# Optimization experiments

Hardware: AMD Instinct MI355X
Metric: run time of the kernel (lower is better)

The kernel has to match this reference:

```python
import jax, jax.numpy as jnp
import numpy as np

N_NODES = 100000
N_EDGES = 3200000
IN_F, HID, OUT = 3, 32, 1
NEG_SLOPE = 0.2


def _glorot(key, shape):
    fan_in, fan_out = shape[0], shape[-1]
    lim = jnp.sqrt(6.0 / (fan_in + fan_out)).astype(jnp.float32)
    return jax.random.uniform(key, shape, jnp.float32, -lim, lim)


def setup_inputs() -> dict:
    key = jax.random.key(0)
    ks = jax.random.split(key, 12)
    x = jax.random.normal(ks[0], (N_NODES, IN_F), jnp.float32)
    edge_index = jax.random.randint(ks[1], (2, N_EDGES), 0, N_NODES, jnp.int32)
    return {
        "x": x,
        "edge_index": edge_index,
        "W1": _glorot(ks[2], (IN_F, HID)),
        "att_src1": _glorot(ks[3], (1, HID))[0],
        "att_dst1": _glorot(ks[4], (1, HID))[0],
        "b1": jnp.zeros((HID,), jnp.float32),
        "W2": _glorot(ks[5], (HID, HID)),
        "att_src2": _glorot(ks[6], (1, HID))[0],
        "att_dst2": _glorot(ks[7], (1, HID))[0],
        "b2": jnp.zeros((HID,), jnp.float32),
        "Wl": _glorot(ks[8], (HID, OUT)),
        "bl": jnp.zeros((OUT,), jnp.float32),
    }


def gat_layer(x, src, dst, W, att_src, att_dst, b):
    # h: [N, HID] dense transform
    h = x @ W
    # per-node attention halves (compute once per node, gather per edge)
    a_s = h @ att_src  # [N]
    a_d = h @ att_dst  # [N]
    logits = jax.nn.leaky_relu(a_s[src] + a_d[dst], NEG_SLOPE)  # [E+N]
    # segment-softmax over incoming edges of each dst node
    m = jax.ops.segment_max(logits, dst, num_segments=N_NODES)
    m = jnp.where(jnp.isfinite(m), m, 0.0)
    ex = jnp.exp(logits - m[dst])
    denom = jax.ops.segment_sum(ex, dst, num_segments=N_NODES)
    coef = ex / (denom[dst] + 1e-16)
    # weighted scatter-aggregate of source messages
    out = jax.ops.segment_sum(coef[:, None] * h[src], dst, num_segments=N_NODES)
    return out + b


def reference(x, edge_index, W1, att_src1, att_dst1, b1, W2, att_src2, att_dst2, b2, Wl, bl):
    # PyG GATConv default: add self-loops
    loops = jnp.arange(N_NODES, dtype=edge_index.dtype)
    src = jnp.concatenate([edge_index[0], loops])
    dst = jnp.concatenate([edge_index[1], loops])
    h = gat_layer(x, src, dst, W1, att_src1, att_dst1, b1)
    h = jax.nn.relu(h)  # dropout is identity in eval
    h = gat_layer(h, src, dst, W2, att_src2, att_dst2, b2)
    h = jax.nn.relu(h)
    return h @ Wl + bl
```

## Files before the change

kernel.cpp:

```cpp
#include <hip/hip_runtime.h>
#include <hip/hip_fp16.h>

#define HID 32
#define BN 132
#define NBPAD 768
#define BSTRIDE 5120
#define CHUNK 4096

__device__ __forceinline__ float lrelu(float x) { return x > 0.0f ? x : 0.2f * x; }

__global__ void k_transform1(const float* __restrict__ x,
                             const float* __restrict__ W1,
                             const float* __restrict__ att_src,
                             const float* __restrict__ att_dst,
                             __half* __restrict__ hh,
                             float* __restrict__ a_s,
                             float* __restrict__ a_d,
                             int* __restrict__ cursor,
                             int N)
{
    int tid = blockIdx.x * blockDim.x + threadIdx.x;
    if (tid < NBPAD) cursor[tid] = 0;
    int n = tid >> 5;
    int f = tid & 31;
    if (n >= N) return;
    float x0 = x[n * 3 + 0], x1 = x[n * 3 + 1], x2 = x[n * 3 + 2];
    float hv = x0 * W1[f] + x1 * W1[HID + f] + x2 * W1[2 * HID + f];
    hh[(size_t)n * HID + f] = __float2half(hv);
    float as = hv * att_src[f];
    float ad = hv * att_dst[f];
    #pragma unroll
    for (int m = 16; m >= 1; m >>= 1) {
        as += __shfl_xor(as, m, 32);
        ad += __shfl_xor(ad, m, 32);
    }
    if (f == 0) { a_s[n] = as; a_d[n] = ad; }
}

__global__ void __launch_bounds__(256) k_binscatter(const int* __restrict__ src,
                                                    const int* __restrict__ dst,
                                                    int* __restrict__ cursor,
                                                    unsigned int* __restrict__ packed,
                                                    int NBr, int E)
{
    __shared__ int stage[CHUNK];
    __shared__ unsigned short sbid[CHUNK];
    __shared__ int lhist[NBPAD], lexcl[NBPAD], lbase[NBPAD], lcur[NBPAD];
    __shared__ int arr[256];
    int t = threadIdx.x;
    for (int i = t; i < NBPAD; i += 256) { lhist[i] = 0; lcur[i] = 0; }
    __syncthreads();
    int base = blockIdx.x * CHUNK;
    int cnt = E - base; if (cnt > CHUNK) cnt = CHUNK;
    for (int i = t; i < cnt; i += 256)
        atomicAdd(&lhist[dst[base + i] / BN], 1);
    __syncthreads();
    int b0 = 3 * t;
    int c0 = lhist[b0], c1 = lhist[b0 + 1], c2 = lhist[b0 + 2];
    int s = c0 + c1 + c2;
    arr[t] = s;
    __syncthreads();
    for (int o = 1; o < 256; o <<= 1) {
        int v = (t >= o) ? arr[t - o] : 0;
        __syncthreads();
        arr[t] += v;
        __syncthreads();
    }
    int ex = arr[t] - s;
    int e0 = ex, e1 = ex + c0, e2 = ex + c0 + c1;
    lexcl[b0] = e0; lexcl[b0 + 1] = e1; lexcl[b0 + 2] = e2;
    for (int i = 0; i < c0; ++i) sbid[e0 + i] = (unsigned short)b0;
    for (int i = 0; i < c1; ++i) sbid[e1 + i] = (unsigned short)(b0 + 1);
    for (int i = 0; i < c2; ++i) sbid[e2 + i] = (unsigned short)(b0 + 2);
    for (int b = t; b < NBr; b += 256)
        if (lhist[b]) lbase[b] = b * BSTRIDE + atomicAdd(&cursor[b], lhist[b]);
    __syncthreads();
    for (int i = t; i < cnt; i += 256) {
        int d = dst[base + i];
        int sv = src[base + i];
        int b = d / BN;
        int dl = d - b * BN;
        int idx = lexcl[b] + atomicAdd(&lcur[b], 1);
        stage[idx] = (int)((unsigned)sv | ((unsigned)dl << 17));
    }
    __syncthreads();
    for (int i = t; i < cnt; i += 256) {
        int b = sbid[i];
        int gpos = lbase[b] + (i - lexcl[b]);
        if (gpos < (b + 1) * BSTRIDE)
            packed[gpos] = (unsigned)stage[i];
    }
}

__device__ __forceinline__ void build_lcsr_exp(const unsigned int* pk, int cnt,
                                               const float* __restrict__ a_s,
                                               const float* __restrict__ a_d,
                                               int nodeBase, int N,
                                               int* lcsr, float* lexp, float* adT,
                                               int* lhist, int* lscan, int* lcur)
{
    int t = threadIdx.x;
    if (t < 256) { lhist[t] = 0; lcur[t] = 0; }
    if (t < BN) {
        int n = nodeBase + t;
        adT[t] = (n < N) ? a_d[n] : 0.0f;
    }
    __syncthreads();
    for (int i = t; i < cnt; i += 512)
        atomicAdd(&lhist[(pk[i] >> 17) & 255], 1);
    __syncthreads();
    if (t < 256) lscan[t] = lhist[t];
    __syncthreads();
    for (int o = 1; o < 256; o <<= 1) {
        int v = (t < 256 && t >= o) ? lscan[t - o] : 0;
        __syncthreads();
        if (t < 256) lscan[t] += v;
        __syncthreads();
    }
    for (int i = t; i < cnt; i += 512) {
        unsigned int p = pk[i];
        int dl = (p >> 17) & 255;
        int sv = (int)(p & 0x1FFFF);
        float e = __expf(lrelu(a_s[sv] + adT[dl]));
        int pos = atomicAdd(&lcur[dl], 1);
        int idx = (lscan[dl] - lhist[dl]) + pos;
        lcsr[idx] = sv;
        lexp[idx] = e;
    }
    __syncthreads();
}

__device__ __forceinline__ void agg_node(const __half* __restrict__ hh,
                                         float ex_self,
                                         const float* __restrict__ b,
                                         int n, int f,
                                         const int* lcsr, const float* lexp,
                                         int off, int dg,
                                         float& vx, float& vy)
{
    float den = ex_self;
    float2 hs = __half22float2(*(const __half2*)(hh + (size_t)n * HID + 2 * f));
    float accx = ex_self * hs.x;
    float accy = ex_self * hs.y;
    int j = 0;
    for (; j + 8 <= dg; j += 8) {
        int s0 = lcsr[off + j + 0], s1 = lcsr[off + j + 1];
        int s2 = lcsr[off + j + 2], s3 = lcsr[off + j + 3];
        int s4 = lcsr[off + j + 4], s5 = lcsr[off + j + 5];
        int s6 = lcsr[off + j + 6], s7 = lcsr[off + j + 7];
        float e0 = lexp[off + j + 0], e1 = lexp[off + j + 1];
        float e2 = lexp[off + j + 2], e3 = lexp[off + j + 3];
        float e4 = lexp[off + j + 4], e5 = lexp[off + j + 5];
        float e6 = lexp[off + j + 6], e7 = lexp[off + j + 7];
        __half2 p0 = *(const __half2*)(hh + (size_t)s0 * HID + 2 * f);
        __half2 p1 = *(const __half2*)(hh + (size_t)s1 * HID + 2 * f);
        __half2 p2 = *(const __half2*)(hh + (size_t)s2 * HID + 2 * f);
        __half2 p3 = *(const __half2*)(hh + (size_t)s3 * HID + 2 * f);
        __half2 p4 = *(const __half2*)(hh + (size_t)s4 * HID + 2 * f);
        __half2 p5 = *(const __half2*)(hh + (size_t)s5 * HID + 2 * f);
        __half2 p6 = *(const __half2*)(hh + (size_t)s6 * HID + 2 * f);
        __half2 p7 = *(const __half2*)(hh + (size_t)s7 * HID + 2 * f);
        float2 q0 = __half22float2(p0), q1 = __half22float2(p1);
        float2 q2 = __half22float2(p2), q3 = __half22float2(p3);
        float2 q4 = __half22float2(p4), q5 = __half22float2(p5);
        float2 q6 = __half22float2(p6), q7 = __half22float2(p7);
        den += ((e0 + e1) + (e2 + e3)) + ((e4 + e5) + (e6 + e7));
        accx = fmaf(e0, q0.x, accx); accy = fmaf(e0, q0.y, accy);
        accx = fmaf(e1, q1.x, accx); accy = fmaf(e1, q1.y, accy);
        accx = fmaf(e2, q2.x, accx); accy = fmaf(e2, q2.y, accy);
        accx = fmaf(e3, q3.x, accx); accy = fmaf(e3, q3.y, accy);
        accx = fmaf(e4, q4.x, accx); accy = fmaf(e4, q4.y, accy);
        accx = fmaf(e5, q5.x, accx); accy = fmaf(e5, q5.y, accy);
        accx = fmaf(e6, q6.x, accx); accy = fmaf(e6, q6.y, accy);
        accx = fmaf(e7, q7.x, accx); accy = fmaf(e7, q7.y, accy);
    }
    for (; j < dg; ++j) {
        int s0 = lcsr[off + j];
        float e0 = lexp[off + j];
        float2 q0 = __half22float2(*(const __half2*)(hh + (size_t)s0 * HID + 2 * f));
        den += e0;
        accx = fmaf(e0, q0.x, accx);
        accy = fmaf(e0, q0.y, accy);
    }
    float inv = 1.0f / (den + 1e-16f);
    vx = fmaxf(accx * inv + b[2 * f], 0.0f);
    vy = fmaxf(accy * inv + b[2 * f + 1], 0.0f);
}

__global__ void __launch_bounds__(512) k_agg_mid_f(const __half* __restrict__ hh,
                          const float* __restrict__ a_s,
                          const float* __restrict__ a_d,
                          const int* __restrict__ cursor,
                          const unsigned int* __restrict__ packed,
                          const float* __restrict__ b1,
                          const float* __restrict__ W2,
                          const float* __restrict__ as2w,
                          const float* __restrict__ ad2w,
                          __half* __restrict__ hh_out,
                          float* __restrict__ as_out,
                          float* __restrict__ ad_out,
                          int N)
{
    __shared__ int lcsr[BSTRIDE];
    __shared__ float lexp[BSTRIDE];
    __shared__ float adT[BN];
    __shared__ int lhist[256], lscan[256], lcur[256];
    int bk = blockIdx.x, t = threadIdx.x;
    int cnt = cursor[bk]; if (cnt > BSTRIDE) cnt = BSTRIDE;
    build_lcsr_exp(packed + (size_t)bk * BSTRIDE, cnt, a_s, a_d, bk * BN, N,
                   lcsr, lexp, adT, lhist, lscan, lcur);
    int g = t >> 4, f = t & 15;
    for (int dl = g; dl < BN; dl += 32) {
        int n = bk * BN + dl;
        if (n >= N) continue;
        int off = lscan[dl] - lhist[dl];
        int dg = lhist[dl];
        float ex_self = __expf(lrelu(a_s[n] + adT[dl]));
        float vx, vy;
        agg_node(hh, ex_self, b1, n, f, lcsr, lexp, off, dg, vx, vy);
        float hx = 0.0f, hy = 0.0f;
        #pragma unroll
        for (int k = 0; k < 16; ++k) {
            float va = __shfl(vx, k, 16);
            float vb = __shfl(vy, k, 16);
            float2 w0 = *(const float2*)(W2 + (2 * k) * HID + 2 * f);
            float2 w1 = *(const float2*)(W2 + (2 * k + 1) * HID + 2 * f);
            hx = fmaf(va, w0.x, hx); hy = fmaf(va, w0.y, hy);
            hx = fmaf(vb, w1.x, hx); hy = fmaf(vb, w1.y, hy);
        }
        *(__half2*)(hh_out + (size_t)n * HID + 2 * f) = __floats2half2_rn(hx, hy);
        float as = hx * as2w[2 * f] + hy * as2w[2 * f + 1];
        float ad = hx * ad2w[2 * f] + hy * ad2w[2 * f + 1];
        #pragma unroll
        for (int m2 = 8; m2 >= 1; m2 >>= 1) {
            as += __shfl_xor(as, m2, 16);
            ad += __shfl_xor(ad, m2, 16);
        }
        if (f == 0) { as_out[n] = as; ad_out[n] = ad; }
    }
}

__global__ void __launch_bounds__(512) k_agg_out_f(const __half* __restrict__ hh,
                          const float* __restrict__ a_s,
                          const float* __restrict__ a_d,
                          const int* __restrict__ cursor,
                          const unsigned int* __restrict__ packed,
                          const float* __restrict__ b2,
                          const float* __restrict__ Wl,
                          const float* __restrict__ bl,
                          float* __restrict__ out,
                          int N)
{
    __shared__ int lcsr[BSTRIDE];
    __shared__ float lexp[BSTRIDE];
    __shared__ float adT[BN];
    __shared__ int lhist[256], lscan[256], lcur[256];
    int bk = blockIdx.x, t = threadIdx.x;
    int cnt = cursor[bk]; if (cnt > BSTRIDE) cnt = BSTRIDE;
    build_lcsr_exp(packed + (size_t)bk * BSTRIDE, cnt, a_s, a_d, bk * BN, N,
                   lcsr, lexp, adT, lhist, lscan, lcur);
    int g = t >> 4, f = t & 15;
    for (int dl = g; dl < BN; dl += 32) {
        int n = bk * BN + dl;
        if (n >= N) continue;
        int off = lscan[dl] - lhist[dl];
        int dg = lhist[dl];
        float ex_self = __expf(lrelu(a_s[n] + adT[dl]));
        float vx, vy;
        agg_node(hh, ex_self, b2, n, f, lcsr, lexp, off, dg, vx, vy);
        float y = vx * Wl[2 * f] + vy * Wl[2 * f + 1];
        #pragma unroll
        for (int m2 = 8; m2 >= 1; m2 >>= 1)
            y += __shfl_xor(y, m2, 16);
        if (f == 0) out[n] = y + bl[0];
    }
}

extern "C" void kernel_launch(void* const* d_in, const int* in_sizes, int n_in,
                              void* d_out, int out_size, void* d_ws, size_t ws_size,
                              hipStream_t stream)
{
    const float* x        = (const float*)d_in[0];
    const int*   eidx     = (const int*)d_in[1];
    const float* W1       = (const float*)d_in[2];
    const float* att_src1 = (const float*)d_in[3];
    const float* att_dst1 = (const float*)d_in[4];
    const float* b1       = (const float*)d_in[5];
    const float* W2       = (const float*)d_in[6];
    const float* att_src2 = (const float*)d_in[7];
    const float* att_dst2 = (const float*)d_in[8];
    const float* b2       = (const float*)d_in[9];
    const float* Wl       = (const float*)d_in[10];
    const float* bl       = (const float*)d_in[11];
    float* out = (float*)d_out;

    int N = in_sizes[0] / 3;
    int E = in_sizes[1] / 2;
    const int* src = eidx;
    const int* dst = eidx + E;
    int NBr = (N + BN - 1) / BN;

    size_t szNHh = (size_t)N * HID * 2;
    size_t szN4  = (size_t)N * 4;
    size_t szPK  = (size_t)NBr * BSTRIDE * 4;

    char* ws = (char*)d_ws;
    __half* h1h    = (__half*)ws; ws += szNHh;
    __half* h2h    = (__half*)ws; ws += szNHh;
    unsigned int* packed = (unsigned int*)ws; ws += szPK;
    float*  a_s1   = (float*)ws;  ws += szN4;
    float*  a_d1   = (float*)ws;  ws += szN4;
    float*  a_s2   = (float*)ws;  ws += szN4;
    float*  a_d2   = (float*)ws;  ws += szN4;
    int*    cursor = (int*)ws;    ws += NBPAD * 4;

    const int B = 256;
    int gridNode32 = (N * HID + B - 1) / B;
    int gridBin    = (E + CHUNK - 1) / CHUNK;

    k_transform1<<<gridNode32, B, 0, stream>>>(x, W1, att_src1, att_dst1,
                                               h1h, a_s1, a_d1, cursor, N);
    k_binscatter<<<gridBin, B, 0, stream>>>(src, dst, cursor, packed, NBr, E);
    k_agg_mid_f<<<NBr, 512, 0, stream>>>(h1h, a_s1, a_d1, cursor, packed,
                                         b1, W2, att_src2, att_dst2,
                                         h2h, a_s2, a_d2, N);
    k_agg_out_f<<<NBr, 512, 0, stream>>>(h2h, a_s2, a_d2, cursor, packed,
                                         b2, Wl, bl, out, N);
}
```

Baseline: 252.3 us.

## Split node features into two half-width arrays and gather in two passes

Stores the 32-wide fp16 hidden features as two separate 16-wide arrays and runs the aggregation as two sequential gather passes, one per half. Partial sums for the first half are kept in shared memory between the passes. The aim is to shrink the working set of each random gather pass (3.2 MB per half) so it stays cache-resident, and to use 8 lanes per node instead of 16. In exchange, the edge list is walked twice per layer, each gather fetches only 32 bytes per row, and the extra shared memory may lower occupancy.

```diff
diff --git a/kernel.cpp b/kernel.cpp
--- a/kernel.cpp
+++ b/kernel.cpp
@@ -2,6 +2,7 @@
 #include <hip/hip_fp16.h>
 
 #define HID 32
+#define HHALF 16
 #define BN 132
 #define NBPAD 768
 #define BSTRIDE 5120
@@ -13,7 +14,8 @@
                              const float* __restrict__ W1,
                              const float* __restrict__ att_src,
                              const float* __restrict__ att_dst,
-                             __half* __restrict__ hh,
+                             __half* __restrict__ hhA,
+                             __half* __restrict__ hhB,
                              float* __restrict__ a_s,
                              float* __restrict__ a_d,
                              int* __restrict__ cursor,
@@ -26,7 +28,8 @@
     if (n >= N) return;
     float x0 = x[n * 3 + 0], x1 = x[n * 3 + 1], x2 = x[n * 3 + 2];
     float hv = x0 * W1[f] + x1 * W1[HID + f] + x2 * W1[2 * HID + f];
-    hh[(size_t)n * HID + f] = __float2half(hv);
+    if (f < HHALF) hhA[(size_t)n * HHALF + f] = __float2half(hv);
+    else           hhB[(size_t)n * HHALF + (f - HHALF)] = __float2half(hv);
     float as = hv * att_src[f];
     float ad = hv * att_dst[f];
     #pragma unroll
@@ -130,18 +133,18 @@
     __syncthreads();
 }
 
-__device__ __forceinline__ void agg_node(const __half* __restrict__ hh,
-                                         float ex_self,
-                                         const float* __restrict__ b,
-                                         int n, int f,
-                                         const int* lcsr, const float* lexp,
-                                         int off, int dg,
-                                         float& vx, float& vy)
-{
-    float den = ex_self;
-    float2 hs = __half22float2(*(const __half2*)(hh + (size_t)n * HID + 2 * f));
-    float accx = ex_self * hs.x;
-    float accy = ex_self * hs.y;
+__device__ __forceinline__ void gather_half(const __half* __restrict__ hhX,
+                                            const int* lcsr, const float* lexp,
+                                            int off, int dg, int f,
+                                            float ex_self, int n,
+                                            bool accDen,
+                                            float& ax, float& ay, float& den)
+{
+    __half2 hs = *(const __half2*)(hhX + (size_t)n * HHALF + 2 * f);
+    float2 q = __half22float2(hs);
+    ax = ex_self * q.x;
+    ay = ex_self * q.y;
+    float d = accDen ? ex_self : 0.0f;
     int j = 0;
     for (; j + 8 <= dg; j += 8) {
         int s0 = lcsr[off + j + 0], s1 = lcsr[off + j + 1];
@@ -152,42 +155,41 @@
         float e2 = lexp[off + j + 2], e3 = lexp[off + j + 3];
         float e4 = lexp[off + j + 4], e5 = lexp[off + j + 5];
         float e6 = lexp[off + j + 6], e7 = lexp[off + j + 7];
-        __half2 p0 = *(const __half2*)(hh + (size_t)s0 * HID + 2 * f);
-        __half2 p1 = *(const __half2*)(hh + (size_t)s1 * HID + 2 * f);
-        __half2 p2 = *(const __half2*)(hh + (size_t)s2 * HID + 2 * f);
-        __half2 p3 = *(const __half2*)(hh + (size_t)s3 * HID + 2 * f);
-        __half2 p4 = *(const __half2*)(hh + (size_t)s4 * HID + 2 * f);
-        __half2 p5 = *(const __half2*)(hh + (size_t)s5 * HID + 2 * f);
-        __half2 p6 = *(const __half2*)(hh + (size_t)s6 * HID + 2 * f);
-        __half2 p7 = *(const __half2*)(hh + (size_t)s7 * HID + 2 * f);
+        __half2 p0 = *(const __half2*)(hhX + (size_t)s0 * HHALF + 2 * f);
+        __half2 p1 = *(const __half2*)(hhX + (size_t)s1 * HHALF + 2 * f);
+        __half2 p2 = *(const __half2*)(hhX + (size_t)s2 * HHALF + 2 * f);
+        __half2 p3 = *(const __half2*)(hhX + (size_t)s3 * HHALF + 2 * f);
+        __half2 p4 = *(const __half2*)(hhX + (size_t)s4 * HHALF + 2 * f);
+        __half2 p5 = *(const __half2*)(hhX + (size_t)s5 * HHALF + 2 * f);
+        __half2 p6 = *(const __half2*)(hhX + (size_t)s6 * HHALF + 2 * f);
+        __half2 p7 = *(const __half2*)(hhX + (size_t)s7 * HHALF + 2 * f);
         float2 q0 = __half22float2(p0), q1 = __half22float2(p1);
         float2 q2 = __half22float2(p2), q3 = __half22float2(p3);
         float2 q4 = __half22float2(p4), q5 = __half22float2(p5);
         float2 q6 = __half22float2(p6), q7 = __half22float2(p7);
-        den += ((e0 + e1) + (e2 + e3)) + ((e4 + e5) + (e6 + e7));
-        accx = fmaf(e0, q0.x, accx); accy = fmaf(e0, q0.y, accy);
-        accx = fmaf(e1, q1.x, accx); accy = fmaf(e1, q1.y, accy);
-        accx = fmaf(e2, q2.x, accx); accy = fmaf(e2, q2.y, accy);
-        accx = fmaf(e3, q3.x, accx); accy = fmaf(e3, q3.y, accy);
-        accx = fmaf(e4, q4.x, accx); accy = fmaf(e4, q4.y, accy);
-        accx = fmaf(e5, q5.x, accx); accy = fmaf(e5, q5.y, accy);
-        accx = fmaf(e6, q6.x, accx); accy = fmaf(e6, q6.y, accy);
-        accx = fmaf(e7, q7.x, accx); accy = fmaf(e7, q7.y, accy);
+        if (accDen) d += ((e0 + e1) + (e2 + e3)) + ((e4 + e5) + (e6 + e7));
+        ax = fmaf(e0, q0.x, ax); ay = fmaf(e0, q0.y, ay);
+        ax = fmaf(e1, q1.x, ax); ay = fmaf(e1, q1.y, ay);
+        ax = fmaf(e2, q2.x, ax); ay = fmaf(e2, q2.y, ay);
+        ax = fmaf(e3, q3.x, ax); ay = fmaf(e3, q3.y, ay);
+        ax = fmaf(e4, q4.x, ax); ay = fmaf(e4, q4.y, ay);
+        ax = fmaf(e5, q5.x, ax); ay = fmaf(e5, q5.y, ay);
+        ax = fmaf(e6, q6.x, ax); ay = fmaf(e6, q6.y, ay);
+        ax = fmaf(e7, q7.x, ax); ay = fmaf(e7, q7.y, ay);
     }
     for (; j < dg; ++j) {
         int s0 = lcsr[off + j];
         float e0 = lexp[off + j];
-        float2 q0 = __half22float2(*(const __half2*)(hh + (size_t)s0 * HID + 2 * f));
-        den += e0;
-        accx = fmaf(e0, q0.x, accx);
-        accy = fmaf(e0, q0.y, accy);
-    }
-    float inv = 1.0f / (den + 1e-16f);
-    vx = fmaxf(accx * inv + b[2 * f], 0.0f);
-    vy = fmaxf(accy * inv + b[2 * f + 1], 0.0f);
-}
-
-__global__ void __launch_bounds__(512) k_agg_mid_f(const __half* __restrict__ hh,
+        float2 q0 = __half22float2(*(const __half2*)(hhX + (size_t)s0 * HHALF + 2 * f));
+        if (accDen) d += e0;
+        ax = fmaf(e0, q0.x, ax);
+        ay = fmaf(e0, q0.y, ay);
+    }
+    if (accDen) den = d;
+}
+
+__global__ void __launch_bounds__(512) k_agg_mid_f(const __half* __restrict__ hhA,
+                          const __half* __restrict__ hhB,
                           const float* __restrict__ a_s,
                           const float* __restrict__ a_d,
                           const int* __restrict__ cursor,
@@ -196,7 +198,8 @@
                           const float* __restrict__ W2,
                           const float* __restrict__ as2w,
                           const float* __restrict__ ad2w,
-                          __half* __restrict__ hh_out,
+                          __half* __restrict__ hhA_out,
+                          __half* __restrict__ hhB_out,
                           float* __restrict__ as_out,
                           float* __restrict__ ad_out,
                           int N)
@@ -204,43 +207,81 @@
     __shared__ int lcsr[BSTRIDE];
     __shared__ float lexp[BSTRIDE];
     __shared__ float adT[BN];
+    __shared__ float accA[BN * HHALF];
+    __shared__ float denB[BN];
     __shared__ int lhist[256], lscan[256], lcur[256];
     int bk = blockIdx.x, t = threadIdx.x;
     int cnt = cursor[bk]; if (cnt > BSTRIDE) cnt = BSTRIDE;
     build_lcsr_exp(packed + (size_t)bk * BSTRIDE, cnt, a_s, a_d, bk * BN, N,
                    lcsr, lexp, adT, lhist, lscan, lcur);
-    int g = t >> 4, f = t & 15;
-    for (int dl = g; dl < BN; dl += 32) {
+    int g = t >> 3, f = t & 7;
+    for (int dl = g; dl < BN; dl += 64) {
         int n = bk * BN + dl;
         if (n >= N) continue;
         int off = lscan[dl] - lhist[dl];
         int dg = lhist[dl];
-        float ex_self = __expf(lrelu(a_s[n] + adT[dl]));
-        float vx, vy;
-        agg_node(hh, ex_self, b1, n, f, lcsr, lexp, off, dg, vx, vy);
-        float hx = 0.0f, hy = 0.0f;
+        float exs = __expf(lrelu(a_s[n] + adT[dl]));
+        float ax, ay, den;
+        gather_half(hhA, lcsr, lexp, off, dg, f, exs, n, true, ax, ay, den);
+        accA[dl * HHALF + 2 * f] = ax;
+        accA[dl * HHALF + 2 * f + 1] = ay;
+        if (f == 0) denB[dl] = den;
+    }
+    __syncthreads();
+    for (int dl = g; dl < BN; dl += 64) {
+        int n = bk * BN + dl;
+        if (n >= N) continue;
+        int off = lscan[dl] - lhist[dl];
+        int dg = lhist[dl];
+        float exs = __expf(lrelu(a_s[n] + adT[dl]));
+        float bx, by, dummy;
+        gather_half(hhB, lcsr, lexp, off, dg, f, exs, n, false, bx, by, dummy);
+        float inv = 1.0f / (denB[dl] + 1e-16f);
+        float vAx = fmaxf(accA[dl * HHALF + 2 * f] * inv + b1[2 * f], 0.0f);
+        float vAy = fmaxf(accA[dl * HHALF + 2 * f + 1] * inv + b1[2 * f + 1], 0.0f);
+        float vBx = fmaxf(bx * inv + b1[HHALF + 2 * f], 0.0f);
+        float vBy = fmaxf(by * inv + b1[HHALF + 2 * f + 1], 0.0f);
+        float oAx = 0.0f, oAy = 0.0f, oBx = 0.0f, oBy = 0.0f;
         #pragma unroll
-        for (int k = 0; k < 16; ++k) {
-            float va = __shfl(vx, k, 16);
-            float vb = __shfl(vy, k, 16);
-            float2 w0 = *(const float2*)(W2 + (2 * k) * HID + 2 * f);
-            float2 w1 = *(const float2*)(W2 + (2 * k + 1) * HID + 2 * f);
-            hx = fmaf(va, w0.x, hx); hy = fmaf(va, w0.y, hy);
-            hx = fmaf(vb, w1.x, hx); hy = fmaf(vb, w1.y, hy);
+        for (int r = 0; r < 8; ++r) {
+            float k0 = __shfl(vAx, r, 8);
+            float k1 = __shfl(vAy, r, 8);
+            float k2 = __shfl(vBx, r, 8);
+            float k3 = __shfl(vBy, r, 8);
+            const float* w0 = W2 + (2 * r) * HID;
+            const float* w1 = W2 + (2 * r + 1) * HID;
+            const float* w2 = W2 + (HHALF + 2 * r) * HID;
+            const float* w3 = W2 + (HHALF + 2 * r + 1) * HID;
+            float2 a0 = *(const float2*)(w0 + 2 * f), c0 = *(const float2*)(w0 + HHALF + 2 * f);
+            float2 a1 = *(const float2*)(w1 + 2 * f), c1 = *(const float2*)(w1 + HHALF + 2 * f);
+            float2 a2 = *(const float2*)(w2 + 2 * f), c2 = *(const float2*)(w2 + HHALF + 2 * f);
+            float2 a3 = *(const float2*)(w3 + 2 * f), c3 = *(const float2*)(w3 + HHALF + 2 * f);
+            oAx = fmaf(k0, a0.x, oAx); oAy = fmaf(k0, a0.y, oAy);
+            oBx = fmaf(k0, c0.x, oBx); oBy = fmaf(k0, c0.y, oBy);
+            oAx = fmaf(k1, a1.x, oAx); oAy = fmaf(k1, a1.y, oAy);
+            oBx = fmaf(k1, c1.x, oBx); oBy = fmaf(k1, c1.y, oBy);
+            oAx = fmaf(k2, a2.x, oAx); oAy = fmaf(k2, a2.y, oAy);
+            oBx = fmaf(k2, c2.x, oBx); oBy = fmaf(k2, c2.y, oBy);
+            oAx = fmaf(k3, a3.x, oAx); oAy = fmaf(k3, a3.y, oAy);
+            oBx = fmaf(k3, c3.x, oBx); oBy = fmaf(k3, c3.y, oBy);
         }
-        *(__half2*)(hh_out + (size_t)n * HID + 2 * f) = __floats2half2_rn(hx, hy);
-        float as = hx * as2w[2 * f] + hy * as2w[2 * f + 1];
-        float ad = hx * ad2w[2 * f] + hy * ad2w[2 * f + 1];
+        *(__half2*)(hhA_out + (size_t)n * HHALF + 2 * f) = __floats2half2_rn(oAx, oAy);
+        *(__half2*)(hhB_out + (size_t)n * HHALF + 2 * f) = __floats2half2_rn(oBx, oBy);
+        float as = oAx * as2w[2 * f] + oAy * as2w[2 * f + 1]
+                 + oBx * as2w[HHALF + 2 * f] + oBy * as2w[HHALF + 2 * f + 1];
+        float ad = oAx * ad2w[2 * f] + oAy * ad2w[2 * f + 1]
+                 + oBx * ad2w[HHALF + 2 * f] + oBy * ad2w[HHALF + 2 * f + 1];
         #pragma unroll
-        for (int m2 = 8; m2 >= 1; m2 >>= 1) {
-            as += __shfl_xor(as, m2, 16);
-            ad += __shfl_xor(ad, m2, 16);
+        for (int m2 = 4; m2 >= 1; m2 >>= 1) {
+            as += __shfl_xor(as, m2, 8);
+            ad += __shfl_xor(ad, m2, 8);
         }
         if (f == 0) { as_out[n] = as; ad_out[n] = ad; }
     }
 }
 
-__global__ void __launch_bounds__(512) k_agg_out_f(const __half* __restrict__ hh,
+__global__ void __launch_bounds__(512) k_agg_out_f(const __half* __restrict__ hhA,
+                          const __half* __restrict__ hhB,
                           const float* __restrict__ a_s,
                           const float* __restrict__ a_d,
                           const int* __restrict__ cursor,
@@ -254,24 +295,45 @@
     __shared__ int lcsr[BSTRIDE];
     __shared__ float lexp[BSTRIDE];
     __shared__ float adT[BN];
+    __shared__ float accA[BN * HHALF];
+    __shared__ float denB[BN];
     __shared__ int lhist[256], lscan[256], lcur[256];
     int bk = blockIdx.x, t = threadIdx.x;
     int cnt = cursor[bk]; if (cnt > BSTRIDE) cnt = BSTRIDE;
     build_lcsr_exp(packed + (size_t)bk * BSTRIDE, cnt, a_s, a_d, bk * BN, N,
                    lcsr, lexp, adT, lhist, lscan, lcur);
-    int g = t >> 4, f = t & 15;
-    for (int dl = g; dl < BN; dl += 32) {
+    int g = t >> 3, f = t & 7;
+    for (int dl = g; dl < BN; dl += 64) {
         int n = bk * BN + dl;
         if (n >= N) continue;
         int off = lscan[dl] - lhist[dl];
         int dg = lhist[dl];
-        float ex_self = __expf(lrelu(a_s[n] + adT[dl]));
-        float vx, vy;
-        agg_node(hh, ex_self, b2, n, f, lcsr, lexp, off, dg, vx, vy);
-        float y = vx * Wl[2 * f] + vy * Wl[2 * f + 1];
+        float exs = __expf(lrelu(a_s[n] + adT[dl]));
+        float ax, ay, den;
+        gather_half(hhA, lcsr, lexp, off, dg, f, exs, n, true, ax, ay, den);
+        accA[dl * HHALF + 2 * f] = ax;
+        accA[dl * HHALF + 2 * f + 1] = ay;
+        if (f == 0) denB[dl] = den;
+    }
+    __syncthreads();
+    for (int dl = g; dl < BN; dl += 64) {
+        int n = bk * BN + dl;
+        if (n >= N) continue;
+        int off = lscan[dl] - lhist[dl];
+        int dg = lhist[dl];
+        float exs = __expf(lrelu(a_s[n] + adT[dl]));
+        float bx, by, dummy;
+        gather_half(hhB, lcsr, lexp, off, dg, f, exs, n, false, bx, by, dummy);
+        float inv = 1.0f / (denB[dl] + 1e-16f);
+        float vAx = fmaxf(accA[dl * HHALF + 2 * f] * inv + b2[2 * f], 0.0f);
+        float vAy = fmaxf(accA[dl * HHALF + 2 * f + 1] * inv + b2[2 * f + 1], 0.0f);
+        float vBx = fmaxf(bx * inv + b2[HHALF + 2 * f], 0.0f);
+        float vBy = fmaxf(by * inv + b2[HHALF + 2 * f + 1], 0.0f);
+        float y = vAx * Wl[2 * f] + vAy * Wl[2 * f + 1]
+                + vBx * Wl[HHALF + 2 * f] + vBy * Wl[HHALF + 2 * f + 1];
         #pragma unroll
-        for (int m2 = 8; m2 >= 1; m2 >>= 1)
-            y += __shfl_xor(y, m2, 16);
+        for (int m2 = 4; m2 >= 1; m2 >>= 1)
+            y += __shfl_xor(y, m2, 8);
         if (f == 0) out[n] = y + bl[0];
     }
 }
@@ -300,13 +362,15 @@
     const int* dst = eidx + E;
     int NBr = (N + BN - 1) / BN;
 
-    size_t szNHh = (size_t)N * HID * 2;
+    size_t szNHf = (size_t)N * HHALF * 2;
     size_t szN4  = (size_t)N * 4;
     size_t szPK  = (size_t)NBr * BSTRIDE * 4;
 
     char* ws = (char*)d_ws;
-    __half* h1h    = (__half*)ws; ws += szNHh;
-    __half* h2h    = (__half*)ws; ws += szNHh;
+    __half* h1A    = (__half*)ws; ws += szNHf;
+    __half* h1B    = (__half*)ws; ws += szNHf;
+    __half* h2A    = (__half*)ws; ws += szNHf;
+    __half* h2B    = (__half*)ws; ws += szNHf;
     unsigned int* packed = (unsigned int*)ws; ws += szPK;
     float*  a_s1   = (float*)ws;  ws += szN4;
     float*  a_d1   = (float*)ws;  ws += szN4;
@@ -319,11 +383,11 @@
     int gridBin    = (E + CHUNK - 1) / CHUNK;
 
     k_transform1<<<gridNode32, B, 0, stream>>>(x, W1, att_src1, att_dst1,
-                                               h1h, a_s1, a_d1, cursor, N);
+                                               h1A, h1B, a_s1, a_d1, cursor, N);
     k_binscatter<<<gridBin, B, 0, stream>>>(src, dst, cursor, packed, NBr, E);
-    k_agg_mid_f<<<NBr, 512, 0, stream>>>(h1h, a_s1, a_d1, cursor, packed,
+    k_agg_mid_f<<<NBr, 512, 0, stream>>>(h1A, h1B, a_s1, a_d1, cursor, packed,
                                          b1, W2, att_src2, att_dst2,
-                                         h2h, a_s2, a_d2, N);
-    k_agg_out_f<<<NBr, 512, 0, stream>>>(h2h, a_s2, a_d2, cursor, packed,
+                                         h2A, h2B, a_s2, a_d2, N);
+    k_agg_out_f<<<NBr, 512, 0, stream>>>(h2A, h2B, a_s2, a_d2, cursor, packed,
                                          b2, Wl, bl, out, N);
 }
```

Result: slower. 268.7 us (+6.5%).

## Fuse all GAT stages into one persistent kernel with grid barriers

Applied to the files above, without the earlier changes.

Replaces the four launches (transform, bin-scatter, two aggregation passes) with one persistent kernel of one block per destination bin. The stages are separated by atomic-counter grid barriers, and a host-side occupancy check falls back to the old path if all blocks cannot be co-resident. Layer 2 reuses the shared-memory CSR built in layer 1 and only recomputes the exponentials, locating each edge's destination by binary search, instead of rebuilding the CSR. BN and BSTRIDE are retuned so the bin count fits under NBPAD. This removes launch gaps and the second CSR build, at the cost of 256-thread aggregation blocks, barrier spin overhead, and reliance on all blocks being resident.

```diff
diff --git a/kernel.cpp b/kernel.cpp
--- a/kernel.cpp
+++ b/kernel.cpp
@@ -2,111 +2,89 @@
 #include <hip/hip_fp16.h>
 
 #define HID 32
-#define BN 132
+#define BN 131
 #define NBPAD 768
-#define BSTRIDE 5120
+#define BSTRIDE 4608
 #define CHUNK 4096
 
 __device__ __forceinline__ float lrelu(float x) { return x > 0.0f ? x : 0.2f * x; }
 
-__global__ void k_transform1(const float* __restrict__ x,
-                             const float* __restrict__ W1,
-                             const float* __restrict__ att_src,
-                             const float* __restrict__ att_dst,
-                             __half* __restrict__ hh,
-                             float* __restrict__ a_s,
-                             float* __restrict__ a_d,
-                             int* __restrict__ cursor,
-                             int N)
-{
-    int tid = blockIdx.x * blockDim.x + threadIdx.x;
-    if (tid < NBPAD) cursor[tid] = 0;
-    int n = tid >> 5;
-    int f = tid & 31;
-    if (n >= N) return;
-    float x0 = x[n * 3 + 0], x1 = x[n * 3 + 1], x2 = x[n * 3 + 2];
-    float hv = x0 * W1[f] + x1 * W1[HID + f] + x2 * W1[2 * HID + f];
-    hh[(size_t)n * HID + f] = __float2half(hv);
-    float as = hv * att_src[f];
-    float ad = hv * att_dst[f];
-    #pragma unroll
-    for (int m = 16; m >= 1; m >>= 1) {
-        as += __shfl_xor(as, m, 32);
-        ad += __shfl_xor(ad, m, 32);
-    }
-    if (f == 0) { a_s[n] = as; a_d[n] = ad; }
-}
-
-__global__ void __launch_bounds__(256) k_binscatter(const int* __restrict__ src,
-                                                    const int* __restrict__ dst,
-                                                    int* __restrict__ cursor,
-                                                    unsigned int* __restrict__ packed,
-                                                    int NBr, int E)
-{
-    __shared__ int stage[CHUNK];
-    __shared__ unsigned short sbid[CHUNK];
-    __shared__ int lhist[NBPAD], lexcl[NBPAD], lbase[NBPAD], lcur[NBPAD];
-    __shared__ int arr[256];
+
+struct BinSM {
+    int stage[CHUNK];
+    unsigned short sbid[CHUNK];
+    int lhist[NBPAD], lexcl[NBPAD], lbase[NBPAD], lcur[NBPAD];
+    int arr[256];
+};
+struct AggSM {
+    int   lcsr[BSTRIDE];
+    float lexp[BSTRIDE];
+    int   lhist[256], lscan[256], lcur[256];
+    float adT[BN];
+};
+union FusedSM { BinSM bin; AggSM agg; };
+
+__device__ __forceinline__ void binscatter_chunk(BinSM& S, int base,
+        const int* __restrict__ src, const int* __restrict__ dst,
+        int* __restrict__ cursor, unsigned int* __restrict__ packed,
+        int NBr, int E)
+{
     int t = threadIdx.x;
-    for (int i = t; i < NBPAD; i += 256) { lhist[i] = 0; lcur[i] = 0; }
-    __syncthreads();
-    int base = blockIdx.x * CHUNK;
+    for (int i = t; i < NBPAD; i += 256) { S.lhist[i] = 0; S.lcur[i] = 0; }
+    __syncthreads();
     int cnt = E - base; if (cnt > CHUNK) cnt = CHUNK;
     for (int i = t; i < cnt; i += 256)
-        atomicAdd(&lhist[dst[base + i] / BN], 1);
+        atomicAdd(&S.lhist[dst[base + i] / BN], 1);
     __syncthreads();
     int b0 = 3 * t;
-    int c0 = lhist[b0], c1 = lhist[b0 + 1], c2 = lhist[b0 + 2];
+    int c0 = S.lhist[b0], c1 = S.lhist[b0 + 1], c2 = S.lhist[b0 + 2];
     int s = c0 + c1 + c2;
-    arr[t] = s;
+    S.arr[t] = s;
     __syncthreads();
     for (int o = 1; o < 256; o <<= 1) {
-        int v = (t >= o) ? arr[t - o] : 0;
+        int v = (t >= o) ? S.arr[t - o] : 0;
         __syncthreads();
-        arr[t] += v;
+        S.arr[t] += v;
         __syncthreads();
     }
-    int ex = arr[t] - s;
+    int ex = S.arr[t] - s;
     int e0 = ex, e1 = ex + c0, e2 = ex + c0 + c1;
-    lexcl[b0] = e0; lexcl[b0 + 1] = e1; lexcl[b0 + 2] = e2;
-    for (int i = 0; i < c0; ++i) sbid[e0 + i] = (unsigned short)b0;
-    for (int i = 0; i < c1; ++i) sbid[e1 + i] = (unsigned short)(b0 + 1);
-    for (int i = 0; i < c2; ++i) sbid[e2 + i] = (unsigned short)(b0 + 2);
+    S.lexcl[b0] = e0; S.lexcl[b0 + 1] = e1; S.lexcl[b0 + 2] = e2;
+    for (int i = 0; i < c0; ++i) S.sbid[e0 + i] = (unsigned short)b0;
+    for (int i = 0; i < c1; ++i) S.sbid[e1 + i] = (unsigned short)(b0 + 1);
+    for (int i = 0; i < c2; ++i) S.sbid[e2 + i] = (unsigned short)(b0 + 2);
     for (int b = t; b < NBr; b += 256)
-        if (lhist[b]) lbase[b] = b * BSTRIDE + atomicAdd(&cursor[b], lhist[b]);
+        if (S.lhist[b]) S.lbase[b] = b * BSTRIDE + atomicAdd(&cursor[b], S.lhist[b]);
     __syncthreads();
     for (int i = t; i < cnt; i += 256) {
         int d = dst[base + i];
         int sv = src[base + i];
         int b = d / BN;
         int dl = d - b * BN;
-        int idx = lexcl[b] + atomicAdd(&lcur[b], 1);
-        stage[idx] = (int)((unsigned)sv | ((unsigned)dl << 17));
+        int idx = S.lexcl[b] + atomicAdd(&S.lcur[b], 1);
+        S.stage[idx] = (int)((unsigned)sv | ((unsigned)dl << 17));
     }
     __syncthreads();
     for (int i = t; i < cnt; i += 256) {
-        int b = sbid[i];
-        int gpos = lbase[b] + (i - lexcl[b]);
+        int b = S.sbid[i];
+        int gpos = S.lbase[b] + (i - S.lexcl[b]);
         if (gpos < (b + 1) * BSTRIDE)
-            packed[gpos] = (unsigned)stage[i];
-    }
-}
-
-__device__ __forceinline__ void build_lcsr_exp(const unsigned int* pk, int cnt,
-                                               const float* __restrict__ a_s,
-                                               const float* __restrict__ a_d,
-                                               int nodeBase, int N,
-                                               int* lcsr, float* lexp, float* adT,
-                                               int* lhist, int* lscan, int* lcur)
+            packed[gpos] = (unsigned)S.stage[i];
+    }
+}
+
+template<int BLK>
+__device__ __forceinline__ void build_csr_exp(int* lcsr, float* lexp, float* adT,
+        int* lhist, int* lscan, int* lcur,
+        const unsigned int* __restrict__ pk, int cnt,
+        const float* __restrict__ a_s, const float* __restrict__ a_d,
+        int nodeBase, int N)
 {
     int t = threadIdx.x;
     if (t < 256) { lhist[t] = 0; lcur[t] = 0; }
-    if (t < BN) {
-        int n = nodeBase + t;
-        adT[t] = (n < N) ? a_d[n] : 0.0f;
-    }
-    __syncthreads();
-    for (int i = t; i < cnt; i += 512)
+    if (t < BN) { int n = nodeBase + t; adT[t] = (n < N) ? a_d[n] : 0.0f; }
+    __syncthreads();
+    for (int i = t; i < cnt; i += BLK)
         atomicAdd(&lhist[(pk[i] >> 17) & 255], 1);
     __syncthreads();
     if (t < 256) lscan[t] = lhist[t];
@@ -117,8 +95,8 @@
         if (t < 256) lscan[t] += v;
         __syncthreads();
     }
-    for (int i = t; i < cnt; i += 512) {
-        unsigned int p = pk[i];
+    for (int i = t; i < cnt; i += BLK) {
+        unsigned p = pk[i];
         int dl = (p >> 17) & 255;
         int sv = (int)(p & 0x1FFFF);
         float e = __expf(lrelu(a_s[sv] + adT[dl]));
@@ -131,12 +109,10 @@
 }
 
 __device__ __forceinline__ void agg_node(const __half* __restrict__ hh,
-                                         float ex_self,
-                                         const float* __restrict__ b,
+                                         float ex_self, const float* __restrict__ b,
                                          int n, int f,
                                          const int* lcsr, const float* lexp,
-                                         int off, int dg,
-                                         float& vx, float& vy)
+                                         int off, int dg, float& vx, float& vy)
 {
     float den = ex_self;
     float2 hs = __half22float2(*(const __half2*)(hh + (size_t)n * HID + 2 * f));
@@ -187,87 +163,224 @@
     vy = fmaxf(accy * inv + b[2 * f + 1], 0.0f);
 }
 
+__device__ __forceinline__ void epi_mid(int n, int f, float vx, float vy,
+        const float* __restrict__ W2, const float* __restrict__ as2w,
+        const float* __restrict__ ad2w,
+        __half* __restrict__ hh_out, float* __restrict__ as_out,
+        float* __restrict__ ad_out)
+{
+    float hx = 0.0f, hy = 0.0f;
+    #pragma unroll
+    for (int k = 0; k < 16; ++k) {
+        float va = __shfl(vx, k, 16);
+        float vb = __shfl(vy, k, 16);
+        float2 w0 = *(const float2*)(W2 + (2 * k) * HID + 2 * f);
+        float2 w1 = *(const float2*)(W2 + (2 * k + 1) * HID + 2 * f);
+        hx = fmaf(va, w0.x, hx); hy = fmaf(va, w0.y, hy);
+        hx = fmaf(vb, w1.x, hx); hy = fmaf(vb, w1.y, hy);
+    }
+    *(__half2*)(hh_out + (size_t)n * HID + 2 * f) = __floats2half2_rn(hx, hy);
+    float as = hx * as2w[2 * f] + hy * as2w[2 * f + 1];
+    float ad = hx * ad2w[2 * f] + hy * ad2w[2 * f + 1];
+    #pragma unroll
+    for (int m2 = 8; m2 >= 1; m2 >>= 1) {
+        as += __shfl_xor(as, m2, 16);
+        ad += __shfl_xor(ad, m2, 16);
+    }
+    if (f == 0) { as_out[n] = as; ad_out[n] = ad; }
+}
+
+__device__ __forceinline__ void grid_bar(int* bar, int target)
+{
+    __syncthreads();
+    if (threadIdx.x == 0) {
+        __threadfence();
+        __hip_atomic_fetch_add(bar, 1, __ATOMIC_RELEASE, __HIP_MEMORY_SCOPE_AGENT);
+        while (__hip_atomic_load(bar, __ATOMIC_ACQUIRE, __HIP_MEMORY_SCOPE_AGENT) < target)
+            __builtin_amdgcn_s_sleep(8);
+        __threadfence();
+    }
+    __syncthreads();
+}
+
+__global__ void k_zero_bar(int* __restrict__ bar)
+{
+    if (threadIdx.x < 4) bar[threadIdx.x] = 0;
+}
+
+__global__ void __launch_bounds__(256) k_fused(
+    const float* __restrict__ x, const int* __restrict__ src, const int* __restrict__ dst,
+    const float* __restrict__ W1, const float* __restrict__ as1w,
+    const float* __restrict__ ad1w, const float* __restrict__ b1,
+    const float* __restrict__ W2, const float* __restrict__ as2w,
+    const float* __restrict__ ad2w, const float* __restrict__ b2,
+    const float* __restrict__ Wl, const float* __restrict__ bl,
+    __half* __restrict__ h1h, __half* __restrict__ h2h,
+    unsigned int* __restrict__ packed,
+    float* __restrict__ a_s1, float* __restrict__ a_d1,
+    float* __restrict__ a_s2, float* __restrict__ a_d2,
+    int* __restrict__ cursor, int* __restrict__ bar,
+    float* __restrict__ out, int N, int E, int NBr)
+{
+    __shared__ FusedSM sm;
+    int t = threadIdx.x, bk = blockIdx.x;
+    int nth = gridDim.x * 256, gtid = bk * 256 + t;
+
+    for (int i = gtid; i < NBPAD; i += nth) cursor[i] = 0;
+    for (int idx = gtid; idx < N * HID; idx += nth) {
+        int n = idx >> 5, f = idx & 31;
+        float x0 = x[n * 3 + 0], x1 = x[n * 3 + 1], x2 = x[n * 3 + 2];
+        float hv = x0 * W1[f] + x1 * W1[HID + f] + x2 * W1[2 * HID + f];
+        h1h[(size_t)n * HID + f] = __float2half(hv);
+        float as = hv * as1w[f];
+        float ad = hv * ad1w[f];
+        #pragma unroll
+        for (int m = 16; m >= 1; m >>= 1) {
+            as += __shfl_xor(as, m, 32);
+            ad += __shfl_xor(ad, m, 32);
+        }
+        if (f == 0) { a_s1[n] = as; a_d1[n] = ad; }
+    }
+    grid_bar(bar, gridDim.x);
+
+    int nch = (E + CHUNK - 1) / CHUNK;
+    for (int c = bk; c < nch; c += gridDim.x) {
+        binscatter_chunk(sm.bin, c * CHUNK, src, dst, cursor, packed, NBr, E);
+        __syncthreads();
+    }
+    grid_bar(bar, 2 * gridDim.x);
+
+    int cnt = cursor[bk]; if (cnt > BSTRIDE) cnt = BSTRIDE;
+    build_csr_exp<256>(sm.agg.lcsr, sm.agg.lexp, sm.agg.adT,
+                       sm.agg.lhist, sm.agg.lscan, sm.agg.lcur,
+                       packed + (size_t)bk * BSTRIDE, cnt, a_s1, a_d1, bk * BN, N);
+    {
+        int g = t >> 4, f = t & 15;
+        for (int dl = g; dl < BN; dl += 16) {
+            int n = bk * BN + dl;
+            if (n >= N) continue;
+            int off = sm.agg.lscan[dl] - sm.agg.lhist[dl];
+            int dg = sm.agg.lhist[dl];
+            float exs = __expf(lrelu(a_s1[n] + sm.agg.adT[dl]));
+            float vx, vy;
+            agg_node(h1h, exs, b1, n, f, sm.agg.lcsr, sm.agg.lexp, off, dg, vx, vy);
+            epi_mid(n, f, vx, vy, W2, as2w, ad2w, h2h, a_s2, a_d2);
+        }
+    }
+    grid_bar(bar, 3 * gridDim.x);
+
+    if (t < BN) { int n = bk * BN + t; sm.agg.adT[t] = (n < N) ? a_d2[n] : 0.0f; }
+    __syncthreads();
+    for (int i = t; i < cnt; i += 256) {
+        int lo = 0, hi = BN - 1;
+        while (lo < hi) {
+            int mid = (lo + hi) >> 1;
+            if (sm.agg.lscan[mid] > i) hi = mid; else lo = mid + 1;
+        }
+        int sv = sm.agg.lcsr[i];
+        sm.agg.lexp[i] = __expf(lrelu(a_s2[sv] + sm.agg.adT[lo]));
+    }
+    __syncthreads();
+    {
+        int g = t >> 4, f = t & 15;
+        for (int dl = g; dl < BN; dl += 16) {
+            int n = bk * BN + dl;
+            if (n >= N) continue;
+            int off = sm.agg.lscan[dl] - sm.agg.lhist[dl];
+            int dg = sm.agg.lhist[dl];
+            float exs = __expf(lrelu(a_s2[n] + sm.agg.adT[dl]));
+            float vx, vy;
+            agg_node(h2h, exs, b2, n, f, sm.agg.lcsr, sm.agg.lexp, off, dg, vx, vy);
+            float y = vx * Wl[2 * f] + vy * Wl[2 * f + 1];
+            #pragma unroll
+            for (int m2 = 8; m2 >= 1; m2 >>= 1)
+                y += __shfl_xor(y, m2, 16);
+            if (f == 0) out[n] = y + bl[0];
+        }
+    }
+}
+
+
+__global__ void k_transform1(const float* __restrict__ x,
+                             const float* __restrict__ W1,
+                             const float* __restrict__ att_src,
+                             const float* __restrict__ att_dst,
+                             __half* __restrict__ hh,
+                             float* __restrict__ a_s,
+                             float* __restrict__ a_d,
+                             int* __restrict__ cursor, int N)
+{
+    int tid = blockIdx.x * blockDim.x + threadIdx.x;
+    if (tid < NBPAD) cursor[tid] = 0;
+    int n = tid >> 5, f = tid & 31;
+    if (n >= N) return;
+    float x0 = x[n * 3 + 0], x1 = x[n * 3 + 1], x2 = x[n * 3 + 2];
+    float hv = x0 * W1[f] + x1 * W1[HID + f] + x2 * W1[2 * HID + f];
+    hh[(size_t)n * HID + f] = __float2half(hv);
+    float as = hv * att_src[f];
+    float ad = hv * att_dst[f];
+    #pragma unroll
+    for (int m = 16; m >= 1; m >>= 1) {
+        as += __shfl_xor(as, m, 32);
+        ad += __shfl_xor(ad, m, 32);
+    }
+    if (f == 0) { a_s[n] = as; a_d[n] = ad; }
+}
+
+__global__ void __launch_bounds__(256) k_binscatter(const int* __restrict__ src,
+        const int* __restrict__ dst, int* __restrict__ cursor,
+        unsigned int* __restrict__ packed, int NBr, int E)
+{
+    __shared__ BinSM S;
+    binscatter_chunk(S, blockIdx.x * CHUNK, src, dst, cursor, packed, NBr, E);
+}
+
 __global__ void __launch_bounds__(512) k_agg_mid_f(const __half* __restrict__ hh,
-                          const float* __restrict__ a_s,
-                          const float* __restrict__ a_d,
-                          const int* __restrict__ cursor,
-                          const unsigned int* __restrict__ packed,
-                          const float* __restrict__ b1,
-                          const float* __restrict__ W2,
-                          const float* __restrict__ as2w,
-                          const float* __restrict__ ad2w,
-                          __half* __restrict__ hh_out,
-                          float* __restrict__ as_out,
-                          float* __restrict__ ad_out,
-                          int N)
-{
-    __shared__ int lcsr[BSTRIDE];
-    __shared__ float lexp[BSTRIDE];
-    __shared__ float adT[BN];
-    __shared__ int lhist[256], lscan[256], lcur[256];
+        const float* __restrict__ a_s, const float* __restrict__ a_d,
+        const int* __restrict__ cursor, const unsigned int* __restrict__ packed,
+        const float* __restrict__ b1, const float* __restrict__ W2,
+        const float* __restrict__ as2w, const float* __restrict__ ad2w,
+        __half* __restrict__ hh_out, float* __restrict__ as_out,
+        float* __restrict__ ad_out, int N)
+{
+    __shared__ AggSM S;
     int bk = blockIdx.x, t = threadIdx.x;
     int cnt = cursor[bk]; if (cnt > BSTRIDE) cnt = BSTRIDE;
-    build_lcsr_exp(packed + (size_t)bk * BSTRIDE, cnt, a_s, a_d, bk * BN, N,
-                   lcsr, lexp, adT, lhist, lscan, lcur);
+    build_csr_exp<512>(S.lcsr, S.lexp, S.adT, S.lhist, S.lscan, S.lcur,
+                       packed + (size_t)bk * BSTRIDE, cnt, a_s, a_d, bk * BN, N);
     int g = t >> 4, f = t & 15;
     for (int dl = g; dl < BN; dl += 32) {
         int n = bk * BN + dl;
         if (n >= N) continue;
-        int off = lscan[dl] - lhist[dl];
-        int dg = lhist[dl];
-        float ex_self = __expf(lrelu(a_s[n] + adT[dl]));
+        int off = S.lscan[dl] - S.lhist[dl];
+        int dg = S.lhist[dl];
+        float exs = __expf(lrelu(a_s[n] + S.adT[dl]));
         float vx, vy;
-        agg_node(hh, ex_self, b1, n, f, lcsr, lexp, off, dg, vx, vy);
-        float hx = 0.0f, hy = 0.0f;
-        #pragma unroll
-        for (int k = 0; k < 16; ++k) {
-            float va = __shfl(vx, k, 16);
-            float vb = __shfl(vy, k, 16);
-            float2 w0 = *(const float2*)(W2 + (2 * k) * HID + 2 * f);
-            float2 w1 = *(const float2*)(W2 + (2 * k + 1) * HID + 2 * f);
-            hx = fmaf(va, w0.x, hx); hy = fmaf(va, w0.y, hy);
-            hx = fmaf(vb, w1.x, hx); hy = fmaf(vb, w1.y, hy);
-        }
-        *(__half2*)(hh_out + (size_t)n * HID + 2 * f) = __floats2half2_rn(hx, hy);
-        float as = hx * as2w[2 * f] + hy * as2w[2 * f + 1];
-        float ad = hx * ad2w[2 * f] + hy * ad2w[2 * f + 1];
-        #pragma unroll
-        for (int m2 = 8; m2 >= 1; m2 >>= 1) {
-            as += __shfl_xor(as, m2, 16);
-            ad += __shfl_xor(ad, m2, 16);
-        }
-        if (f == 0) { as_out[n] = as; ad_out[n] = ad; }
+        agg_node(hh, exs, b1, n, f, S.lcsr, S.lexp, off, dg, vx, vy);
+        epi_mid(n, f, vx, vy, W2, as2w, ad2w, hh_out, as_out, ad_out);
     }
 }
 
 __global__ void __launch_bounds__(512) k_agg_out_f(const __half* __restrict__ hh,
-                          const float* __restrict__ a_s,
-                          const float* __restrict__ a_d,
-                          const int* __restrict__ cursor,
-                          const unsigned int* __restrict__ packed,
-                          const float* __restrict__ b2,
-                          const float* __restrict__ Wl,
-                          const float* __restrict__ bl,
-                          float* __restrict__ out,
-                          int N)
-{
-    __shared__ int lcsr[BSTRIDE];
-    __shared__ float lexp[BSTRIDE];
-    __shared__ float adT[BN];
-    __shared__ int lhist[256], lscan[256], lcur[256];
+        const float* __restrict__ a_s, const float* __restrict__ a_d,
+        const int* __restrict__ cursor, const unsigned int* __restrict__ packed,
+        const float* __restrict__ b2, const float* __restrict__ Wl,
+        const float* __restrict__ bl, float* __restrict__ out, int N)
+{
+    __shared__ AggSM S;
     int bk = blockIdx.x, t = threadIdx.x;
     int cnt = cursor[bk]; if (cnt > BSTRIDE) cnt = BSTRIDE;
-    build_lcsr_exp(packed + (size_t)bk * BSTRIDE, cnt, a_s, a_d, bk * BN, N,
-                   lcsr, lexp, adT, lhist, lscan, lcur);
+    build_csr_exp<512>(S.lcsr, S.lexp, S.adT, S.lhist, S.lscan, S.lcur,
+                       packed + (size_t)bk * BSTRIDE, cnt, a_s, a_d, bk * BN, N);
     int g = t >> 4, f = t & 15;
     for (int dl = g; dl < BN; dl += 32) {
         int n = bk * BN + dl;
         if (n >= N) continue;
-        int off = lscan[dl] - lhist[dl];
-        int dg = lhist[dl];
-        float ex_self = __expf(lrelu(a_s[n] + adT[dl]));
+        int off = S.lscan[dl] - S.lhist[dl];
+        int dg = S.lhist[dl];
+        float exs = __expf(lrelu(a_s[n] + S.adT[dl]));
         float vx, vy;
-        agg_node(hh, ex_self, b2, n, f, lcsr, lexp, off, dg, vx, vy);
+        agg_node(hh, exs, b2, n, f, S.lcsr, S.lexp, off, dg, vx, vy);
         float y = vx * Wl[2 * f] + vy * Wl[2 * f + 1];
         #pragma unroll
         for (int m2 = 8; m2 >= 1; m2 >>= 1)
@@ -313,17 +426,33 @@
     float*  a_s2   = (float*)ws;  ws += szN4;
     float*  a_d2   = (float*)ws;  ws += szN4;
     int*    cursor = (int*)ws;    ws += NBPAD * 4;
-
-    const int B = 256;
-    int gridNode32 = (N * HID + B - 1) / B;
-    int gridBin    = (E + CHUNK - 1) / CHUNK;
-
-    k_transform1<<<gridNode32, B, 0, stream>>>(x, W1, att_src1, att_dst1,
-                                               h1h, a_s1, a_d1, cursor, N);
-    k_binscatter<<<gridBin, B, 0, stream>>>(src, dst, cursor, packed, NBr, E);
-    k_agg_mid_f<<<NBr, 512, 0, stream>>>(h1h, a_s1, a_d1, cursor, packed,
-                                         b1, W2, att_src2, att_dst2,
-                                         h2h, a_s2, a_d2, N);
-    k_agg_out_f<<<NBr, 512, 0, stream>>>(h2h, a_s2, a_d2, cursor, packed,
-                                         b2, Wl, bl, out, N);
-}
+    int*    bar    = (int*)ws;    ws += 64;
+
+    int dev = 0, cus = 0, maxb = 0;
+    hipGetDevice(&dev);
+    hipDeviceGetAttribute(&cus, hipDeviceAttributeMultiprocessorCount, dev);
+    hipOccupancyMaxActiveBlocksPerMultiprocessor(&maxb, k_fused, 256, 0);
+    bool fused_ok = ((long)maxb * (long)cus >= (long)NBr) && (NBr <= NBPAD);
+
+    if (fused_ok) {
+        k_zero_bar<<<1, 64, 0, stream>>>(bar);
+        k_fused<<<NBr, 256, 0, stream>>>(x, src, dst,
+                                         W1, att_src1, att_dst1, b1,
+                                         W2, att_src2, att_dst2, b2,
+                                         Wl, bl, h1h, h2h, packed,
+                                         a_s1, a_d1, a_s2, a_d2,
+                                         cursor, bar, out, N, E, NBr);
+    } else {
+        const int B = 256;
+        int gridNode32 = (N * HID + B - 1) / B;
+        int gridBin    = (E + CHUNK - 1) / CHUNK;
+        k_transform1<<<gridNode32, B, 0, stream>>>(x, W1, att_src1, att_dst1,
+                                                   h1h, a_s1, a_d1, cursor, N);
+        k_binscatter<<<gridBin, B, 0, stream>>>(src, dst, cursor, packed, NBr, E);
+        k_agg_mid_f<<<NBr, 512, 0, stream>>>(h1h, a_s1, a_d1, cursor, packed,
+                                             b1, W2, att_src2, att_dst2,
+                                             h2h, a_s2, a_d2, N);
+        k_agg_out_f<<<NBr, 512, 0, stream>>>(h2h, a_s2, a_d2, cursor, packed,
+                                             b2, Wl, bl, out, N);
+    }
+}
```

Measured after the change: 249.9 us. No clear change (-1.0%).
